# Kernel optimization log

Hardware: AMD Instinct MI355X
Metric: run time of the kernel (lower is better)

## Reference

```python
import jax, jax.numpy as jnp
import numpy as np

N_U, N_O = 20000, 10000      # rows in users / orders
C = 256                      # channels
TXT = 1536                   # text_embed_dim
NNUM, NCAT, NTXT = 3, 3, 1   # columns per stype (same for both tables)
NCOLS = NNUM + NCAT + NTXT   # 7 columns per table
VOCAB = 101                  # num_cats + 1
E = 10000                    # edges (orders -> users fkey)
MAXP = 16                    # max_parents


def setup_inputs() -> dict:
    key = jax.random.key(0)
    ks = jax.random.split(key, 24)
    s = 0.02
    return {
        "users_num": jax.random.normal(ks[0], (N_U, NNUM), jnp.float32),
        "users_cat": jax.random.randint(ks[1], (N_U, NCAT), 0, VOCAB),
        "users_text": jax.random.normal(ks[2], (N_U, NTXT, TXT), jnp.float32),
        "orders_num": jax.random.normal(ks[3], (N_O, NNUM), jnp.float32),
        "orders_cat": jax.random.randint(ks[4], (N_O, NCAT), 0, VOCAB),
        "orders_text": jax.random.normal(ks[5], (N_O, NTXT, TXT), jnp.float32),
        "edge_index": jax.random.randint(ks[6], (2, E), 0, N_O),
        "table_emb": jax.random.normal(ks[7], (2, C), jnp.float32) * s,
        # users params
        "u_num_w": jax.random.normal(ks[8], (NNUM, C), jnp.float32) * s,
        "u_num_b": jax.random.normal(ks[9], (NNUM, C), jnp.float32) * s,
        "u_cat_tab": jax.random.normal(ks[10], (NCAT, VOCAB, C), jnp.float32) * s,
        "u_txt_w": jax.random.normal(ks[11], (NTXT, C, TXT), jnp.float32) * s,
        "u_txt_b": jax.random.normal(ks[12], (NTXT, C), jnp.float32) * s,
        "u_col": jax.random.normal(ks[13], (NCOLS, C), jnp.float32) * s,
        # orders params
        "o_num_w": jax.random.normal(ks[14], (NNUM, C), jnp.float32) * s,
        "o_num_b": jax.random.normal(ks[15], (NNUM, C), jnp.float32) * s,
        "o_cat_tab": jax.random.normal(ks[16], (NCAT, VOCAB, C), jnp.float32) * s,
        "o_txt_w": jax.random.normal(ks[17], (NTXT, C, TXT), jnp.float32) * s,
        "o_txt_b": jax.random.normal(ks[18], (NTXT, C), jnp.float32) * s,
        "o_col": jax.random.normal(ks[19], (NCOLS, C), jnp.float32) * s,
    }


def _table_tokens(num, cat, txt, nw, nb, ctab, tw, tb, col, temb):
    # num: [N, NNUM]; nw/nb: [NNUM, C] -> per-col Linear(1, C) + SiLU
    tn = jax.nn.silu(num[:, :, None] * nw[None] + nb[None])        # [N, NNUM, C]
    # per-col Embedding lookup: ctab [NCAT, V, C], cat [N, NCAT]
    tc = ctab[jnp.arange(ctab.shape[0])[None, :], cat]             # [N, NCAT, C]
    # per-col Linear(TXT, C): tw [NTXT, C, TXT]
    tt = jnp.einsum('nkt,kct->nkc', txt, tw) + tb[None]            # [N, NTXT, C]
    tok = jnp.concatenate([tn, tc, tt], axis=1) + col[None] + temb  # [N, NCOLS, C]
    # original concatenates per-column blocks of N rows each -> (cols, N, C) flatten
    return tok.transpose(1, 0, 2).reshape(-1, tok.shape[-1])


def reference(users_num, users_cat, users_text, orders_num, orders_cat, orders_text,
              edge_index, table_emb,
              u_num_w, u_num_b, u_cat_tab, u_txt_w, u_txt_b, u_col,
              o_num_w, o_num_b, o_cat_tab, o_txt_w, o_txt_b, o_col):
    xu = _table_tokens(users_num, users_cat, users_text,
                       u_num_w, u_num_b, u_cat_tab, u_txt_w, u_txt_b, u_col, table_emb[0])
    xo = _table_tokens(orders_num, orders_cat, orders_text,
                       o_num_w, o_num_b, o_cat_tab, o_txt_w, o_txt_b, o_col, table_emb[1])
    x = jnp.concatenate([xu, xo], axis=0)                           # [S, C]

    node_idxs = jnp.concatenate([jnp.tile(jnp.arange(N_U), NCOLS),
                                 jnp.tile(jnp.arange(N_U, N_U + N_O), NCOLS)])
    col_idxs = jnp.concatenate([jnp.repeat(jnp.arange(NCOLS), N_U),
                                jnp.repeat(jnp.arange(NCOLS, 2 * NCOLS), N_O)])
    table_idxs = jnp.concatenate([jnp.zeros(NCOLS * N_U, jnp.int32),
                                  jnp.ones(NCOLS * N_O, jnp.int32)])

    # f2p neighbor build: first MAXP parents per child node, in edge order
    num_nodes = N_U + N_O
    child = edge_index[0] + N_U    # orders offset = N_U
    parent = edge_index[1]         # users offset = 0
    order = jnp.argsort(child, stable=True)
    cs, ps = child[order], parent[order]
    seg_start = jnp.searchsorted(cs, cs, side='left')
    rank = jnp.arange(E) - seg_start                                # position within child's group
    valid = rank < MAXP
    tbl = jnp.full((num_nodes + 1, MAXP), -1, dtype=ps.dtype)
    tbl = tbl.at[jnp.where(valid, cs, num_nodes), jnp.minimum(rank, MAXP - 1)].set(
        jnp.where(valid, ps, -1))
    f2p_nbr_idxs = tbl[:num_nodes][node_idxs]                       # [S, MAXP]

    return (x, node_idxs, col_idxs, table_idxs, f2p_nbr_idxs, num_nodes)
```

## Files before the change

### kernel.cpp

```cpp
#include <hip/hip_runtime.h>
#include <hip/hip_bf16.h>

typedef __bf16 bf16;
typedef __bf16 bf16x8 __attribute__((ext_vector_type(8)));
typedef float f32x4 __attribute__((ext_vector_type(4)));

#define NU 20000
#define NO 10000
#define CDIM 256
#define TDIM 1536
#define EN 10000
#define VOCAB 101
#define MAXP 16
#define CAP 32

#define NODE_OFF 53760000LL
#define COL_OFF  53970000LL
#define TAB_OFF  54180000LL
#define F2P_OFF  54390000LL
#define NN_OFF   57750000LL

#define GEMM_U_BLKS 314
#define GEMM_O_BLKS 158
#define MISC_BLKS   22500
#define IDX_BLKS    840
#define MISC_OFF    (GEMM_U_BLKS + GEMM_O_BLKS)
#define IDX_OFF     (MISC_OFF + MISC_BLKS)
#define TOTAL_BLKS  (IDX_OFF + IDX_BLKS)

#define P_EDGE  40
#define P_CVU   (P_EDGE + 7500)
#define P_CVO   (P_CVU + 3750)
#define P_CVWU  (P_CVO + 96)
#define P_CVWO  (P_CVWU + 96)
#define PREP_BLKS P_CVWO

#define WS_PAIRS_OFF 65536ULL
#define WS_TBL_OFF   (WS_PAIRS_OFF + (unsigned long long)NO * CAP * 8)
#define WS_AB_U_OFF  (WS_TBL_OFF + (unsigned long long)NO * MAXP * 4)
#define WS_AB_O_OFF  (WS_AB_U_OFF + (unsigned long long)NU * TDIM * 2)
#define WS_WB_U_OFF  (WS_AB_O_OFF + (unsigned long long)NO * TDIM * 2)
#define WS_WB_O_OFF  (WS_WB_U_OFF + (unsigned long long)CDIM * TDIM * 2)
#define WS_NEED      (WS_WB_O_OFF + (unsigned long long)CDIM * TDIM * 2)

__device__ __forceinline__ void edges_body(int eblk, const int* __restrict__ edge,
                                           int* __restrict__ counts,
                                           unsigned long long* __restrict__ pairs)
{
    int e = eblk * 256 + threadIdx.x;
    if (e >= EN) return;
    int child = edge[e];
    unsigned parent = (unsigned)edge[EN + e];
    int slot = atomicAdd(&counts[child], 1);
    if (slot < CAP)
        pairs[child * CAP + slot] = ((unsigned long long)(unsigned)e << 32) | parent;
}

__global__ void build_tbl(const int* __restrict__ counts,
                          const unsigned long long* __restrict__ pairs,
                          int* __restrict__ tbl)
{
    int mm = blockIdx.x * 256 + threadIdx.x;
    if (mm >= NO) return;
    int cnt = counts[mm];
    if (cnt > CAP) cnt = CAP;
    unsigned long long v[CAP];
    for (int i = 0; i < cnt; i++) v[i] = pairs[mm * CAP + i];
    for (int i = 1; i < cnt; i++) {
        unsigned long long key = v[i];
        int j = i - 1;
        while (j >= 0 && v[j] > key) { v[j + 1] = v[j]; j--; }
        v[j + 1] = key;
    }
#pragma unroll
    for (int j = 0; j < MAXP; j++)
        tbl[mm * MAXP + j] = (j < cnt) ? (int)(v[j] & 0xffffffffULL) : -1;
}

__device__ __forceinline__ void conv_body(const float* __restrict__ src,
                                          bf16* __restrict__ dst, int relblk)
{
    long long e = (long long)relblk * 4096 + (long long)threadIdx.x * 16;
    float4 f0 = *(const float4*)&src[e];
    float4 f1 = *(const float4*)&src[e + 4];
    float4 f2 = *(const float4*)&src[e + 8];
    float4 f3 = *(const float4*)&src[e + 12];
    bf16x8 h0 = {(bf16)f0.x, (bf16)f0.y, (bf16)f0.z, (bf16)f0.w,
                 (bf16)f1.x, (bf16)f1.y, (bf16)f1.z, (bf16)f1.w};
    bf16x8 h1 = {(bf16)f2.x, (bf16)f2.y, (bf16)f2.z, (bf16)f2.w,
                 (bf16)f3.x, (bf16)f3.y, (bf16)f3.z, (bf16)f3.w};
    *(bf16x8*)&dst[e]     = h0;
    *(bf16x8*)&dst[e + 8] = h1;
}

__global__ __launch_bounds__(256) void prep(
    const int* __restrict__ edge, int* __restrict__ counts,
    unsigned long long* __restrict__ pairs,
    const float* __restrict__ users_text, const float* __restrict__ orders_text,
    const float* __restrict__ utw, const float* __restrict__ otw,
    bf16* __restrict__ AbU, bf16* __restrict__ AbO,
    bf16* __restrict__ WbU, bf16* __restrict__ WbO)
{
    int b = blockIdx.x;
    if (b < P_EDGE)       edges_body(b, edge, counts, pairs);
    else if (b < P_CVU)   conv_body(users_text,  AbU, b - P_EDGE);
    else if (b < P_CVO)   conv_body(orders_text, AbO, b - P_CVU);
    else if (b < P_CVWU)  conv_body(utw, WbU, b - P_CVO);
    else                  conv_body(otw, WbO, b - P_CVWU);
}

__device__ __forceinline__ void idx_body(int iblk, const int* __restrict__ tbl,
                                         float* __restrict__ out)
{
    int i = iblk * 256 + threadIdx.x;
    if (i >= 210000) return;
    float nodev, colvf, tabv;
    int m = -1;
    if (i < 140000) {
        int n = i % 20000;
        nodev = (float)n; colvf = (float)(i / 20000); tabv = 0.f;
    } else {
        int i2 = i - 140000;
        m = i2 % 10000;
        nodev = (float)(20000 + m); colvf = (float)(7 + i2 / 10000); tabv = 1.f;
    }
    out[NODE_OFF + i] = nodev;
    out[COL_OFF + i]  = colvf;
    out[TAB_OFF + i]  = tabv;

    float h[16];
    if (m < 0) {
#pragma unroll
        for (int j = 0; j < 16; j++) h[j] = -1.f;
    } else {
#pragma unroll
        for (int j = 0; j < 16; j++) h[j] = (float)tbl[m * MAXP + j];
    }
    float4* dst = (float4*)&out[F2P_OFF + (long long)i * 16];
#pragma unroll
    for (int j = 0; j < 4; j++)
        dst[j] = *(const float4*)&h[j * 4];
    if (i == 0) out[NN_OFF] = 30000.f;
}

__device__ __forceinline__ void misc_body(int mb,
    const float* __restrict__ unum, const int* __restrict__ ucat,
    const float* __restrict__ onum, const int* __restrict__ ocat,
    const float* __restrict__ temb,
    const float* __restrict__ unw, const float* __restrict__ unb,
    const float* __restrict__ uctab, const float* __restrict__ ucol,
    const float* __restrict__ onw, const float* __restrict__ onb,
    const float* __restrict__ octab, const float* __restrict__ ocol,
    float* __restrict__ out)
{
    int t = threadIdx.x;
    int ridx = mb * 8 + (t >> 5);
    int c0 = (t & 31) * 8;
    bool isU = ridx < 120000;
    int k, n; long long orow;
    const float *num, *nw, *nb, *ctab, *colw, *te;
    const int* cat;
    if (isU) {
        k = ridx / 20000; n = ridx - k * 20000; orow = ridx;
        num = unum; cat = ucat; nw = unw; nb = unb; ctab = uctab; colw = ucol; te = temb;
    } else {
        int i2 = ridx - 120000;
        k = i2 / 10000; n = i2 - k * 10000; orow = (long long)ridx + 20000;
        num = onum; cat = ocat; nw = onw; nb = onb; ctab = octab; colw = ocol; te = temb + CDIM;
    }
    float colv[8], tev[8];
    *(float4*)&colv[0] = *(const float4*)&colw[k * CDIM + c0];
    *(float4*)&colv[4] = *(const float4*)&colw[k * CDIM + c0 + 4];
    *(float4*)&tev[0]  = *(const float4*)&te[c0];
    *(float4*)&tev[4]  = *(const float4*)&te[c0 + 4];
    float res[8];
    if (k < 3) {
        float v = num[n * 3 + k];
        float wv[8], bv[8];
        *(float4*)&wv[0] = *(const float4*)&nw[k * CDIM + c0];
        *(float4*)&wv[4] = *(const float4*)&nw[k * CDIM + c0 + 4];
        *(float4*)&bv[0] = *(const float4*)&nb[k * CDIM + c0];
        *(float4*)&bv[4] = *(const float4*)&nb[k * CDIM + c0 + 4];
#pragma unroll
        for (int j = 0; j < 8; j++) {
            float x = v * wv[j] + bv[j];
            float s = x / (1.f + __expf(-x));
            res[j] = s + colv[j] + tev[j];
        }
    } else {
        int cv = cat[n * 3 + (k - 3)];
        float tcv[8];
        *(float4*)&tcv[0] = *(const float4*)&ctab[((k - 3) * VOCAB + cv) * CDIM + c0];
        *(float4*)&tcv[4] = *(const float4*)&ctab[((k - 3) * VOCAB + cv) * CDIM + c0 + 4];
#pragma unroll
        for (int j = 0; j < 8; j++)
            res[j] = tcv[j] + colv[j] + tev[j];
    }
    *(float4*)&out[orow * CDIM + c0]     = *(const float4*)&res[0];
    *(float4*)&out[orow * CDIM + c0 + 4] = *(const float4*)&res[4];
}

__device__ __forceinline__ void gload16(const void* g, void* l)
{
    __builtin_amdgcn_global_load_lds(
        (const __attribute__((address_space(1))) void*)g,
        (__attribute__((address_space(3))) void*)l, 16, 0, 0);
}

__device__ __forceinline__ void gemm_bf16_body(
    const bf16* __restrict__ A, const bf16* __restrict__ W,
    const float* __restrict__ tbias, const float* __restrict__ colw,
    const float* __restrict__ temb, float* __restrict__ out,
    int M, long long out_row_base, int mblk, int nblk,
    bf16* As, bf16* Bs)
{
    const int tid = threadIdx.x;
    const int m0 = mblk * 128;
    const int n0 = nblk * 128;
    const int w = tid >> 6, lane = tid & 63;
    const int wm = (w & 1) * 64, wn = (w >> 1) * 64;
    const int lrow = lane & 15, lquad = lane >> 4;

    f32x4 acc[4][4];
#pragma unroll
    for (int a = 0; a < 4; a++)
#pragma unroll
        for (int b = 0; b < 4; b++) acc[a][b] = (f32x4){0.f, 0.f, 0.f, 0.f};

    for (int k0 = 0; k0 < TDIM; k0 += 64) {
        __syncthreads();
#pragma unroll
        for (int i = 0; i < 4; i++) {
            int ch = i * 256 + w * 64 + lane;
            int row = ch >> 3, col8 = (ch & 7) * 8;
            int ga = m0 + row; if (ga >= M) ga = M - 1;
            gload16(&A[(size_t)ga * TDIM + k0 + col8], &As[(size_t)(i * 256 + w * 64) * 8]);
            gload16(&W[(size_t)(n0 + row) * TDIM + k0 + col8], &Bs[(size_t)(i * 256 + w * 64) * 8]);
        }
        __syncthreads();
#pragma unroll
        for (int ks = 0; ks < 2; ks++) {
            bf16x8 afr[4], bfr[4];
#pragma unroll
            for (int mi = 0; mi < 4; mi++)
                afr[mi] = *(const bf16x8*)&As[(wm + mi * 16 + lrow) * 64 + ks * 32 + lquad * 8];
#pragma unroll
            for (int ni = 0; ni < 4; ni++)
                bfr[ni] = *(const bf16x8*)&Bs[(wn + ni * 16 + lrow) * 64 + ks * 32 + lquad * 8];
#pragma unroll
            for (int mi = 0; mi < 4; mi++)
#pragma unroll
                for (int ni = 0; ni < 4; ni++)
                    acc[mi][ni] = __builtin_amdgcn_mfma_f32_16x16x32_bf16(
                        afr[mi], bfr[ni], acc[mi][ni], 0, 0, 0);
        }
    }

#pragma unroll
    for (int ni = 0; ni < 4; ni++) {
        int c = n0 + wn + ni * 16 + lrow;
        float bias = tbias[c] + colw[6 * CDIM + c] + temb[c];
#pragma unroll
        for (int mi = 0; mi < 4; mi++) {
            int mbase = m0 + wm + mi * 16 + lquad * 4;
#pragma unroll
            for (int r = 0; r < 4; r++) {
                int m = mbase + r;
                if (m < M)
                    out[(out_row_base + m) * CDIM + c] = acc[mi][ni][r] + bias;
            }
        }
    }
}

__device__ __forceinline__ void gemm_f32_body(
    const float* __restrict__ A, const float* __restrict__ W,
    const float* __restrict__ tbias, const float* __restrict__ colw,
    const float* __restrict__ temb, float* __restrict__ out,
    int M, long long out_row_base, int mblk, int nblk,
    bf16* As, bf16* Bs)
{
    constexpr int LDA = 72;
    const int tid = threadIdx.x;
    const int m0 = mblk * 128;
    const int n0 = nblk * 128;
    const int w = tid >> 6, lane = tid & 63;
    const int wm = (w & 1) * 64, wn = (w >> 1) * 64;
    const int lrow = lane & 15, lquad = lane >> 4;

    f32x4 acc[4][4];
#pragma unroll
    for (int a = 0; a < 4; a++)
#pragma unroll
        for (int b = 0; b < 4; b++) acc[a][b] = (f32x4){0.f, 0.f, 0.f, 0.f};

    for (int k0 = 0; k0 < TDIM; k0 += 64) {
        __syncthreads();
#pragma unroll
        for (int i = 0; i < 8; i++) {
            int c = tid + i * 256;
            int row = c >> 4;
            int col4 = (c & 15) << 2;
            int ga = m0 + row; if (ga >= M) ga = M - 1;
            float4 av = *(const float4*)&A[(size_t)ga * TDIM + k0 + col4];
            __attribute__((aligned(8))) bf16 ha[4] =
                {(bf16)av.x, (bf16)av.y, (bf16)av.z, (bf16)av.w};
            *(unsigned long long*)&As[row * LDA + col4] = *(const unsigned long long*)ha;
            float4 bv = *(const float4*)&W[(size_t)(n0 + row) * TDIM + k0 + col4];
            __attribute__((aligned(8))) bf16 hb[4] =
                {(bf16)bv.x, (bf16)bv.y, (bf16)bv.z, (bf16)bv.w};
            *(unsigned long long*)&Bs[row * LDA + col4] = *(const unsigned long long*)hb;
        }
        __syncthreads();
#pragma unroll
        for (int ks = 0; ks < 2; ks++) {
            bf16x8 afr[4], bfr[4];
#pragma unroll
            for (int mi = 0; mi < 4; mi++)
                afr[mi] = *(const bf16x8*)&As[(wm + mi * 16 + lrow) * LDA + ks * 32 + lquad * 8];
#pragma unroll
            for (int ni = 0; ni < 4; ni++)
                bfr[ni] = *(const bf16x8*)&Bs[(wn + ni * 16 + lrow) * LDA + ks * 32 + lquad * 8];
#pragma unroll
            for (int mi = 0; mi < 4; mi++)
#pragma unroll
                for (int ni = 0; ni < 4; ni++)
                    acc[mi][ni] = __builtin_amdgcn_mfma_f32_16x16x32_bf16(
                        afr[mi], bfr[ni], acc[mi][ni], 0, 0, 0);
        }
    }

#pragma unroll
    for (int ni = 0; ni < 4; ni++) {
        int c = n0 + wn + ni * 16 + lrow;
        float bias = tbias[c] + colw[6 * CDIM + c] + temb[c];
#pragma unroll
        for (int mi = 0; mi < 4; mi++) {
            int mbase = m0 + wm + mi * 16 + lquad * 4;
#pragma unroll
            for (int r = 0; r < 4; r++) {
                int m = mbase + r;
                if (m < M)
                    out[(out_row_base + m) * CDIM + c] = acc[mi][ni][r] + bias;
            }
        }
    }
}

__global__ __launch_bounds__(256) void mega(
    const float* __restrict__ users_num, const int* __restrict__ users_cat,
    const float* __restrict__ orders_num, const int* __restrict__ orders_cat,
    const float* __restrict__ temb,
    const float* __restrict__ unw, const float* __restrict__ unb,
    const float* __restrict__ uctab,
    const float* __restrict__ utb, const float* __restrict__ ucol,
    const float* __restrict__ onw, const float* __restrict__ onb,
    const float* __restrict__ octab,
    const float* __restrict__ otb, const float* __restrict__ ocol,
    const bf16* __restrict__ AbU, const bf16* __restrict__ AbO,
    const bf16* __restrict__ WbU, const bf16* __restrict__ WbO,
    const int* __restrict__ tbl, float* __restrict__ out)
{
    __shared__ bf16 As[128 * 64];
    __shared__ bf16 Bs[128 * 64];
    int b = blockIdx.x;
    if (b < GEMM_U_BLKS) {
        gemm_bf16_body(AbU, WbU, utb, ucol, temb, out,
                       NU, 120000LL, b >> 1, b & 1, As, Bs);
    } else if (b < MISC_OFF) {
        int bb = b - GEMM_U_BLKS;
        gemm_bf16_body(AbO, WbO, otb, ocol, temb + CDIM, out,
                       NO, 200000LL, bb >> 1, bb & 1, As, Bs);
    } else if (b < IDX_OFF) {
        misc_body(b - MISC_OFF, users_num, users_cat, orders_num, orders_cat,
                  temb, unw, unb, uctab, ucol, onw, onb, octab, ocol, out);
    } else {
        idx_body(b - IDX_OFF, tbl, out);
    }
}

__global__ __launch_bounds__(256) void mega_fb(
    const float* __restrict__ users_num, const int* __restrict__ users_cat,
    const float* __restrict__ users_text,
    const float* __restrict__ orders_num, const int* __restrict__ orders_cat,
    const float* __restrict__ orders_text,
    const float* __restrict__ temb,
    const float* __restrict__ unw, const float* __restrict__ unb,
    const float* __restrict__ uctab, const float* __restrict__ utw,
    const float* __restrict__ utb, const float* __restrict__ ucol,
    const float* __restrict__ onw, const float* __restrict__ onb,
    const float* __restrict__ octab, const float* __restrict__ otw,
    const float* __restrict__ otb, const float* __restrict__ ocol,
    const int* __restrict__ tbl, float* __restrict__ out)
{
    __shared__ bf16 As[128 * 72];
    __shared__ bf16 Bs[128 * 72];
    int b = blockIdx.x;
    if (b < GEMM_U_BLKS) {
        gemm_f32_body(users_text, utw, utb, ucol, temb, out,
                      NU, 120000LL, b >> 1, b & 1, As, Bs);
    } else if (b < MISC_OFF) {
        int bb = b - GEMM_U_BLKS;
        gemm_f32_body(orders_text, otw, otb, ocol, temb + CDIM, out,
                      NO, 200000LL, bb >> 1, bb & 1, As, Bs);
    } else if (b < IDX_OFF) {
        misc_body(b - MISC_OFF, users_num, users_cat, orders_num, orders_cat,
                  temb, unw, unb, uctab, ucol, onw, onb, octab, ocol, out);
    } else {
        idx_body(b - IDX_OFF, tbl, out);
    }
}

__global__ void edges_fill(const int* __restrict__ edge, int* __restrict__ counts,
                           unsigned long long* __restrict__ pairs)
{
    edges_body(blockIdx.x, edge, counts, pairs);
}

extern "C" void kernel_launch(void* const* d_in, const int* in_sizes, int n_in,
                              void* d_out, int out_size, void* d_ws, size_t ws_size,
                              hipStream_t stream)
{
    const float* users_num   = (const float*)d_in[0];
    const int*   users_cat   = (const int*)d_in[1];
    const float* users_text  = (const float*)d_in[2];
    const float* orders_num  = (const float*)d_in[3];
    const int*   orders_cat  = (const int*)d_in[4];
    const float* orders_text = (const float*)d_in[5];
    const int*   edge_index  = (const int*)d_in[6];
    const float* table_emb   = (const float*)d_in[7];
    const float* u_num_w   = (const float*)d_in[8];
    const float* u_num_b   = (const float*)d_in[9];
    const float* u_cat_tab = (const float*)d_in[10];
    const float* u_txt_w   = (const float*)d_in[11];
    const float* u_txt_b   = (const float*)d_in[12];
    const float* u_col     = (const float*)d_in[13];
    const float* o_num_w   = (const float*)d_in[14];
    const float* o_num_b   = (const float*)d_in[15];
    const float* o_cat_tab = (const float*)d_in[16];
    const float* o_txt_w   = (const float*)d_in[17];
    const float* o_txt_b   = (const float*)d_in[18];
    const float* o_col     = (const float*)d_in[19];
    float* out = (float*)d_out;

    int* counts = (int*)d_ws;
    unsigned long long* pairs = (unsigned long long*)((char*)d_ws + WS_PAIRS_OFF);
    int* tbl = (int*)((char*)d_ws + WS_TBL_OFF);

    hipMemsetAsync(counts, 0, NO * sizeof(int), stream);

    if (ws_size >= WS_NEED) {
        bf16* AbU = (bf16*)((char*)d_ws + WS_AB_U_OFF);
        bf16* AbO = (bf16*)((char*)d_ws + WS_AB_O_OFF);
        bf16* WbU = (bf16*)((char*)d_ws + WS_WB_U_OFF);
        bf16* WbO = (bf16*)((char*)d_ws + WS_WB_O_OFF);
        prep<<<PREP_BLKS, 256, 0, stream>>>(edge_index, counts, pairs,
            users_text, orders_text, u_txt_w, o_txt_w, AbU, AbO, WbU, WbO);
        build_tbl<<<(NO + 255) / 256, 256, 0, stream>>>(counts, pairs, tbl);
        mega<<<TOTAL_BLKS, 256, 0, stream>>>(
            users_num, users_cat, orders_num, orders_cat,
            table_emb, u_num_w, u_num_b, u_cat_tab, u_txt_b, u_col,
            o_num_w, o_num_b, o_cat_tab, o_txt_b, o_col,
            AbU, AbO, WbU, WbO, tbl, out);
    } else {
        edges_fill<<<P_EDGE, 256, 0, stream>>>(edge_index, counts, pairs);
        build_tbl<<<(NO + 255) / 256, 256, 0, stream>>>(counts, pairs, tbl);
        mega_fb<<<TOTAL_BLKS, 256, 0, stream>>>(
            users_num, users_cat, users_text, orders_num, orders_cat, orders_text,
            table_emb, u_num_w, u_num_b, u_cat_tab, u_txt_w, u_txt_b, u_col,
            o_num_w, o_num_b, o_cat_tab, o_txt_w, o_txt_b, o_col, tbl, out);
    }
}
```

Baseline: 493.2 us.

## Convert text activations to bf16 inside GEMM and pre-swizzle weights

Drops the separate prep pass that converted the text activations to bf16 in workspace. The GEMM now reads the fp32 text directly, converts it in registers and stores it into a padded shared-memory tile. Weights are converted once with an XOR-swizzled layout so async loads avoid bank conflicts. The misc and index bodies also process four rows per block to cut block count. The cost is that A loads become synchronous register loads instead of direct-to-LDS async copies, plus extra conversion work inside the GEMM loop.

```diff
diff --git a/kernel.cpp b/kernel.cpp
--- a/kernel.cpp
+++ b/kernel.cpp
@@ -22,24 +22,20 @@
 
 #define GEMM_U_BLKS 314
 #define GEMM_O_BLKS 158
-#define MISC_BLKS   22500
-#define IDX_BLKS    840
+#define MISC_BLKS   5625
+#define IDX_BLKS    206
 #define MISC_OFF    (GEMM_U_BLKS + GEMM_O_BLKS)
 #define IDX_OFF     (MISC_OFF + MISC_BLKS)
 #define TOTAL_BLKS  (IDX_OFF + IDX_BLKS)
 
 #define P_EDGE  40
-#define P_CVU   (P_EDGE + 7500)
-#define P_CVO   (P_CVU + 3750)
-#define P_CVWU  (P_CVO + 96)
+#define P_CVWU  (P_EDGE + 96)
 #define P_CVWO  (P_CVWU + 96)
 #define PREP_BLKS P_CVWO
 
 #define WS_PAIRS_OFF 65536ULL
 #define WS_TBL_OFF   (WS_PAIRS_OFF + (unsigned long long)NO * CAP * 8)
-#define WS_AB_U_OFF  (WS_TBL_OFF + (unsigned long long)NO * MAXP * 4)
-#define WS_AB_O_OFF  (WS_AB_U_OFF + (unsigned long long)NU * TDIM * 2)
-#define WS_WB_U_OFF  (WS_AB_O_OFF + (unsigned long long)NO * TDIM * 2)
+#define WS_WB_U_OFF  (WS_TBL_OFF + (unsigned long long)NO * MAXP * 4)
 #define WS_WB_O_OFF  (WS_WB_U_OFF + (unsigned long long)CDIM * TDIM * 2)
 #define WS_NEED      (WS_WB_O_OFF + (unsigned long long)CDIM * TDIM * 2)
 
@@ -77,10 +73,16 @@
         tbl[mm * MAXP + j] = (j < cnt) ? (int)(v[j] & 0xffffffffULL) : -1;
 }
 
-__device__ __forceinline__ void conv_body(const float* __restrict__ src,
-                                          bf16* __restrict__ dst, int relblk)
-{
-    long long e = (long long)relblk * 4096 + (long long)threadIdx.x * 16;
+__device__ __forceinline__ void conv_w_body(const float* __restrict__ src,
+                                            bf16* __restrict__ dst, int relblk)
+{
+    int t = threadIdx.x;
+    long long e = (long long)relblk * 4096 + (long long)t * 16;
+    int row = (int)(e / TDIM);
+    int col = (int)(e - (long long)row * TDIM);
+    int kb = col >> 6;
+    int cc = (col & 63) >> 3;
+    int x = row & 7;
     float4 f0 = *(const float4*)&src[e];
     float4 f1 = *(const float4*)&src[e + 4];
     float4 f2 = *(const float4*)&src[e + 8];
@@ -89,58 +91,58 @@
                  (bf16)f1.x, (bf16)f1.y, (bf16)f1.z, (bf16)f1.w};
     bf16x8 h1 = {(bf16)f2.x, (bf16)f2.y, (bf16)f2.z, (bf16)f2.w,
                  (bf16)f3.x, (bf16)f3.y, (bf16)f3.z, (bf16)f3.w};
-    *(bf16x8*)&dst[e]     = h0;
-    *(bf16x8*)&dst[e + 8] = h1;
+    long long base = (long long)row * TDIM + kb * 64;
+    *(bf16x8*)&dst[base + ((cc ^ x) * 8)]       = h0;
+    *(bf16x8*)&dst[base + (((cc + 1) ^ x) * 8)] = h1;
 }
 
 __global__ __launch_bounds__(256) void prep(
     const int* __restrict__ edge, int* __restrict__ counts,
     unsigned long long* __restrict__ pairs,
-    const float* __restrict__ users_text, const float* __restrict__ orders_text,
     const float* __restrict__ utw, const float* __restrict__ otw,
-    bf16* __restrict__ AbU, bf16* __restrict__ AbO,
     bf16* __restrict__ WbU, bf16* __restrict__ WbO)
 {
     int b = blockIdx.x;
     if (b < P_EDGE)       edges_body(b, edge, counts, pairs);
-    else if (b < P_CVU)   conv_body(users_text,  AbU, b - P_EDGE);
-    else if (b < P_CVO)   conv_body(orders_text, AbO, b - P_CVU);
-    else if (b < P_CVWU)  conv_body(utw, WbU, b - P_CVO);
-    else                  conv_body(otw, WbO, b - P_CVWU);
+    else if (b < P_CVWU)  conv_w_body(utw, WbU, b - P_EDGE);
+    else                  conv_w_body(otw, WbO, b - P_CVWU);
 }
 
 __device__ __forceinline__ void idx_body(int iblk, const int* __restrict__ tbl,
                                          float* __restrict__ out)
 {
-    int i = iblk * 256 + threadIdx.x;
-    if (i >= 210000) return;
-    float nodev, colvf, tabv;
-    int m = -1;
-    if (i < 140000) {
-        int n = i % 20000;
-        nodev = (float)n; colvf = (float)(i / 20000); tabv = 0.f;
-    } else {
-        int i2 = i - 140000;
-        m = i2 % 10000;
-        nodev = (float)(20000 + m); colvf = (float)(7 + i2 / 10000); tabv = 1.f;
-    }
-    out[NODE_OFF + i] = nodev;
-    out[COL_OFF + i]  = colvf;
-    out[TAB_OFF + i]  = tabv;
-
-    float h[16];
-    if (m < 0) {
-#pragma unroll
-        for (int j = 0; j < 16; j++) h[j] = -1.f;
-    } else {
-#pragma unroll
-        for (int j = 0; j < 16; j++) h[j] = (float)tbl[m * MAXP + j];
-    }
-    float4* dst = (float4*)&out[F2P_OFF + (long long)i * 16];
-#pragma unroll
-    for (int j = 0; j < 4; j++)
-        dst[j] = *(const float4*)&h[j * 4];
-    if (i == 0) out[NN_OFF] = 30000.f;
+#pragma unroll
+    for (int it = 0; it < 4; it++) {
+        int i = iblk * 1024 + it * 256 + threadIdx.x;
+        if (i >= 210000) return;
+        float nodev, colvf, tabv;
+        int m = -1;
+        if (i < 140000) {
+            int n = i % 20000;
+            nodev = (float)n; colvf = (float)(i / 20000); tabv = 0.f;
+        } else {
+            int i2 = i - 140000;
+            m = i2 % 10000;
+            nodev = (float)(20000 + m); colvf = (float)(7 + i2 / 10000); tabv = 1.f;
+        }
+        out[NODE_OFF + i] = nodev;
+        out[COL_OFF + i]  = colvf;
+        out[TAB_OFF + i]  = tabv;
+
+        float h[16];
+        if (m < 0) {
+#pragma unroll
+            for (int j = 0; j < 16; j++) h[j] = -1.f;
+        } else {
+#pragma unroll
+            for (int j = 0; j < 16; j++) h[j] = (float)tbl[m * MAXP + j];
+        }
+        float4* dst = (float4*)&out[F2P_OFF + (long long)i * 16];
+#pragma unroll
+        for (int j = 0; j < 4; j++)
+            dst[j] = *(const float4*)&h[j * 4];
+        if (i == 0) out[NN_OFF] = 30000.f;
+    }
 }
 
 __device__ __forceinline__ void misc_body(int mb,
@@ -154,50 +156,53 @@
     float* __restrict__ out)
 {
     int t = threadIdx.x;
-    int ridx = mb * 8 + (t >> 5);
     int c0 = (t & 31) * 8;
-    bool isU = ridx < 120000;
-    int k, n; long long orow;
-    const float *num, *nw, *nb, *ctab, *colw, *te;
-    const int* cat;
-    if (isU) {
-        k = ridx / 20000; n = ridx - k * 20000; orow = ridx;
-        num = unum; cat = ucat; nw = unw; nb = unb; ctab = uctab; colw = ucol; te = temb;
-    } else {
-        int i2 = ridx - 120000;
-        k = i2 / 10000; n = i2 - k * 10000; orow = (long long)ridx + 20000;
-        num = onum; cat = ocat; nw = onw; nb = onb; ctab = octab; colw = ocol; te = temb + CDIM;
-    }
-    float colv[8], tev[8];
-    *(float4*)&colv[0] = *(const float4*)&colw[k * CDIM + c0];
-    *(float4*)&colv[4] = *(const float4*)&colw[k * CDIM + c0 + 4];
-    *(float4*)&tev[0]  = *(const float4*)&te[c0];
-    *(float4*)&tev[4]  = *(const float4*)&te[c0 + 4];
-    float res[8];
-    if (k < 3) {
-        float v = num[n * 3 + k];
-        float wv[8], bv[8];
-        *(float4*)&wv[0] = *(const float4*)&nw[k * CDIM + c0];
-        *(float4*)&wv[4] = *(const float4*)&nw[k * CDIM + c0 + 4];
-        *(float4*)&bv[0] = *(const float4*)&nb[k * CDIM + c0];
-        *(float4*)&bv[4] = *(const float4*)&nb[k * CDIM + c0 + 4];
-#pragma unroll
-        for (int j = 0; j < 8; j++) {
-            float x = v * wv[j] + bv[j];
-            float s = x / (1.f + __expf(-x));
-            res[j] = s + colv[j] + tev[j];
-        }
-    } else {
-        int cv = cat[n * 3 + (k - 3)];
-        float tcv[8];
-        *(float4*)&tcv[0] = *(const float4*)&ctab[((k - 3) * VOCAB + cv) * CDIM + c0];
-        *(float4*)&tcv[4] = *(const float4*)&ctab[((k - 3) * VOCAB + cv) * CDIM + c0 + 4];
-#pragma unroll
-        for (int j = 0; j < 8; j++)
-            res[j] = tcv[j] + colv[j] + tev[j];
-    }
-    *(float4*)&out[orow * CDIM + c0]     = *(const float4*)&res[0];
-    *(float4*)&out[orow * CDIM + c0 + 4] = *(const float4*)&res[4];
+#pragma unroll
+    for (int it = 0; it < 4; it++) {
+        int ridx = mb * 32 + it * 8 + (t >> 5);
+        bool isU = ridx < 120000;
+        int k, n; long long orow;
+        const float *num, *nw, *nb, *ctab, *colw, *te;
+        const int* cat;
+        if (isU) {
+            k = ridx / 20000; n = ridx - k * 20000; orow = ridx;
+            num = unum; cat = ucat; nw = unw; nb = unb; ctab = uctab; colw = ucol; te = temb;
+        } else {
+            int i2 = ridx - 120000;
+            k = i2 / 10000; n = i2 - k * 10000; orow = (long long)ridx + 20000;
+            num = onum; cat = ocat; nw = onw; nb = onb; ctab = octab; colw = ocol; te = temb + CDIM;
+        }
+        float colv[8], tev[8];
+        *(float4*)&colv[0] = *(const float4*)&colw[k * CDIM + c0];
+        *(float4*)&colv[4] = *(const float4*)&colw[k * CDIM + c0 + 4];
+        *(float4*)&tev[0]  = *(const float4*)&te[c0];
+        *(float4*)&tev[4]  = *(const float4*)&te[c0 + 4];
+        float res[8];
+        if (k < 3) {
+            float v = num[n * 3 + k];
+            float wv[8], bv[8];
+            *(float4*)&wv[0] = *(const float4*)&nw[k * CDIM + c0];
+            *(float4*)&wv[4] = *(const float4*)&nw[k * CDIM + c0 + 4];
+            *(float4*)&bv[0] = *(const float4*)&nb[k * CDIM + c0];
+            *(float4*)&bv[4] = *(const float4*)&nb[k * CDIM + c0 + 4];
+#pragma unroll
+            for (int j = 0; j < 8; j++) {
+                float x = v * wv[j] + bv[j];
+                float s = x / (1.f + __expf(-x));
+                res[j] = s + colv[j] + tev[j];
+            }
+        } else {
+            int cv = cat[n * 3 + (k - 3)];
+            float tcv[8];
+            *(float4*)&tcv[0] = *(const float4*)&ctab[((k - 3) * VOCAB + cv) * CDIM + c0];
+            *(float4*)&tcv[4] = *(const float4*)&ctab[((k - 3) * VOCAB + cv) * CDIM + c0 + 4];
+#pragma unroll
+            for (int j = 0; j < 8; j++)
+                res[j] = tcv[j] + colv[j] + tev[j];
+        }
+        *(float4*)&out[orow * CDIM + c0]     = *(const float4*)&res[0];
+        *(float4*)&out[orow * CDIM + c0 + 4] = *(const float4*)&res[4];
+    }
 }
 
 __device__ __forceinline__ void gload16(const void* g, void* l)
@@ -207,12 +212,12 @@
         (__attribute__((address_space(3))) void*)l, 16, 0, 0);
 }
 
-__device__ __forceinline__ void gemm_bf16_body(
-    const bf16* __restrict__ A, const bf16* __restrict__ W,
+__device__ __forceinline__ void gemm_hyb_body(
+    const float* __restrict__ A, const bf16* __restrict__ Wswz,
     const float* __restrict__ tbias, const float* __restrict__ colw,
     const float* __restrict__ temb, float* __restrict__ out,
     int M, long long out_row_base, int mblk, int nblk,
-    bf16* As, bf16* Bs)
+    bf16* As , bf16* Bs )
 {
     const int tid = threadIdx.x;
     const int m0 = mblk * 128;
@@ -220,6 +225,7 @@
     const int w = tid >> 6, lane = tid & 63;
     const int wm = (w & 1) * 64, wn = (w >> 1) * 64;
     const int lrow = lane & 15, lquad = lane >> 4;
+    const int bxor = lrow & 7;
 
     f32x4 acc[4][4];
 #pragma unroll
@@ -232,10 +238,19 @@
 #pragma unroll
         for (int i = 0; i < 4; i++) {
             int ch = i * 256 + w * 64 + lane;
-            int row = ch >> 3, col8 = (ch & 7) * 8;
+            int row = ch >> 3, c8 = (ch & 7) * 8;
+            gload16(&Wswz[(size_t)(n0 + row) * TDIM + k0 + c8],
+                    &Bs[(size_t)(i * 256 + w * 64) * 8]);
+        }
+#pragma unroll
+        for (int i = 0; i < 8; i++) {
+            int c = tid + i * 256;
+            int row = c >> 4, col4 = (c & 15) << 2;
             int ga = m0 + row; if (ga >= M) ga = M - 1;
-            gload16(&A[(size_t)ga * TDIM + k0 + col8], &As[(size_t)(i * 256 + w * 64) * 8]);
-            gload16(&W[(size_t)(n0 + row) * TDIM + k0 + col8], &Bs[(size_t)(i * 256 + w * 64) * 8]);
+            float4 av = *(const float4*)&A[(size_t)ga * TDIM + k0 + col4];
+            __attribute__((aligned(8))) bf16 ha[4] =
+                {(bf16)av.x, (bf16)av.y, (bf16)av.z, (bf16)av.w};
+            *(unsigned long long*)&As[row * 72 + col4] = *(const unsigned long long*)ha;
         }
         __syncthreads();
 #pragma unroll
@@ -243,10 +258,11 @@
             bf16x8 afr[4], bfr[4];
 #pragma unroll
             for (int mi = 0; mi < 4; mi++)
-                afr[mi] = *(const bf16x8*)&As[(wm + mi * 16 + lrow) * 64 + ks * 32 + lquad * 8];
+                afr[mi] = *(const bf16x8*)&As[(wm + mi * 16 + lrow) * 72 + ks * 32 + lquad * 8];
 #pragma unroll
             for (int ni = 0; ni < 4; ni++)
-                bfr[ni] = *(const bf16x8*)&Bs[(wn + ni * 16 + lrow) * 64 + ks * 32 + lquad * 8];
+                bfr[ni] = *(const bf16x8*)&Bs[(wn + ni * 16 + lrow) * 64 +
+                                              (((ks * 4 + lquad) ^ bxor) * 8)];
 #pragma unroll
             for (int mi = 0; mi < 4; mi++)
 #pragma unroll
@@ -349,7 +365,9 @@
 
 __global__ __launch_bounds__(256) void mega(
     const float* __restrict__ users_num, const int* __restrict__ users_cat,
+    const float* __restrict__ users_text,
     const float* __restrict__ orders_num, const int* __restrict__ orders_cat,
+    const float* __restrict__ orders_text,
     const float* __restrict__ temb,
     const float* __restrict__ unw, const float* __restrict__ unb,
     const float* __restrict__ uctab,
@@ -357,20 +375,19 @@
     const float* __restrict__ onw, const float* __restrict__ onb,
     const float* __restrict__ octab,
     const float* __restrict__ otb, const float* __restrict__ ocol,
-    const bf16* __restrict__ AbU, const bf16* __restrict__ AbO,
     const bf16* __restrict__ WbU, const bf16* __restrict__ WbO,
     const int* __restrict__ tbl, float* __restrict__ out)
 {
-    __shared__ bf16 As[128 * 64];
+    __shared__ bf16 As[128 * 72];
     __shared__ bf16 Bs[128 * 64];
     int b = blockIdx.x;
     if (b < GEMM_U_BLKS) {
-        gemm_bf16_body(AbU, WbU, utb, ucol, temb, out,
-                       NU, 120000LL, b >> 1, b & 1, As, Bs);
+        gemm_hyb_body(users_text, WbU, utb, ucol, temb, out,
+                      NU, 120000LL, b >> 1, b & 1, As, Bs);
     } else if (b < MISC_OFF) {
         int bb = b - GEMM_U_BLKS;
-        gemm_bf16_body(AbO, WbO, otb, ocol, temb + CDIM, out,
-                       NO, 200000LL, bb >> 1, bb & 1, As, Bs);
+        gemm_hyb_body(orders_text, WbO, otb, ocol, temb + CDIM, out,
+                      NO, 200000LL, bb >> 1, bb & 1, As, Bs);
     } else if (b < IDX_OFF) {
         misc_body(b - MISC_OFF, users_num, users_cat, orders_num, orders_cat,
                   temb, unw, unb, uctab, ucol, onw, onb, octab, ocol, out);
@@ -450,18 +467,16 @@
     hipMemsetAsync(counts, 0, NO * sizeof(int), stream);
 
     if (ws_size >= WS_NEED) {
-        bf16* AbU = (bf16*)((char*)d_ws + WS_AB_U_OFF);
-        bf16* AbO = (bf16*)((char*)d_ws + WS_AB_O_OFF);
         bf16* WbU = (bf16*)((char*)d_ws + WS_WB_U_OFF);
         bf16* WbO = (bf16*)((char*)d_ws + WS_WB_O_OFF);
         prep<<<PREP_BLKS, 256, 0, stream>>>(edge_index, counts, pairs,
-            users_text, orders_text, u_txt_w, o_txt_w, AbU, AbO, WbU, WbO);
+                                            u_txt_w, o_txt_w, WbU, WbO);
         build_tbl<<<(NO + 255) / 256, 256, 0, stream>>>(counts, pairs, tbl);
         mega<<<TOTAL_BLKS, 256, 0, stream>>>(
-            users_num, users_cat, orders_num, orders_cat,
+            users_num, users_cat, users_text, orders_num, orders_cat, orders_text,
             table_emb, u_num_w, u_num_b, u_cat_tab, u_txt_b, u_col,
             o_num_w, o_num_b, o_cat_tab, o_txt_b, o_col,
-            AbU, AbO, WbU, WbO, tbl, out);
+            WbU, WbO, tbl, out);
     } else {
         edges_fill<<<P_EDGE, 256, 0, stream>>>(edge_index, counts, pairs);
         build_tbl<<<(NO + 255) / 256, 256, 0, stream>>>(counts, pairs, tbl);
```

Measured after the change: 457.3 us. 7.3% less time.
